# Performance work log

Measured on AMD Instinct MI355X. Metric: run time of the kernel, lower is better.

The kernel has to match this reference:

```python
import jax, jax.numpy as jnp
import numpy as np

KERNEL_SIZE = 16
STRIDE = 8
NEG = -1.0e9


def setup_inputs() -> dict:
    key = jax.random.key(0)
    k1, k2, k3, k4, k5 = jax.random.split(key, 5)
    B, C, L = 8, 512, 4096
    x = jax.random.normal(k1, (B, C, L), dtype=jnp.float32)
    mask = jax.random.randint(k2, (B, L), 0, 2).astype(bool)
    W = jax.random.normal(k3, (C, C), dtype=jnp.float32) * 0.02
    b = jax.random.normal(k4, (C,), dtype=jnp.float32) * 0.02
    v = jax.random.normal(k5, (C,), dtype=jnp.float32) * 0.02
    return {"x": x, "mask": mask, "W": W, "b": b, "v": v}


def reference(x, mask, W, b, v):
    # x: [B, C, L], mask: [B, L] (True = masked out)
    B, C, L = x.shape
    win, step = KERNEL_SIZE, STRIDE
    L_pool = 1 + (L - win) // step
    # per-token projection (identical across windows since proj is per-token)
    h = jnp.tanh(jnp.einsum('bcl,dc->bld', x, W) + b)      # [B, L, C]
    s = jnp.einsum('bld,d->bl', h, v)                       # [B, L]
    idx = jnp.arange(L_pool)[:, None] * step + jnp.arange(win)[None, :]
    sw = s[:, idx]
    mw = mask[:, idx]
    sw = jnp.where(mw, NEG, sw)
    w = jax.nn.softmax(sw, axis=-1)
    w = jnp.where(mw, 0.0, w)
    norm = jnp.clip(jnp.sum(w, axis=-1, keepdims=True), 1e-6, None)
    w = w / norm
    xw = x[:, :, idx]
    return jnp.einsum('bcpw,bpw->bcp', xw, w)               # [B, C, L_pool]
```

## Files before the change

kernel.cpp:

```cpp
#include <hip/hip_runtime.h>
#include <hip/hip_bf16.h>
#include <cmath>

#define Bsz 8
#define Csz 512
#define Lsz 4096
#define LPOOL 511
#define NEGV -1000000000.0f

typedef __attribute__((ext_vector_type(8))) short short8;
typedef __attribute__((ext_vector_type(4))) float float4v;

__device__ __forceinline__ float bf2f(short u) {
  unsigned int x = ((unsigned int)(unsigned short)u) << 16;
  return __builtin_bit_cast(float, x);
}

__device__ __forceinline__ void gl_lds16(const __hip_bfloat16* g, void* l) {
  __builtin_amdgcn_global_load_lds(
      (const __attribute__((address_space(1))) unsigned int*)g,
      (__attribute__((address_space(3))) unsigned int*)l, 16, 0, 0);
}

__global__ __launch_bounds__(256) void stage1(const float* __restrict__ x,
    __hip_bfloat16* __restrict__ xTs, __hip_bfloat16* __restrict__ xbf,
    const unsigned char* __restrict__ mb, int* __restrict__ flag,
    float* __restrict__ s, const float* __restrict__ W,
    __hip_bfloat16* __restrict__ Wts) {
  const int tid = threadIdx.x;
  const int bid = blockIdx.x;
  if (bid < 4096) {
    __shared__ float sX[64][65];
    const int lt = bid & 63, ct = (bid >> 6) & 7, b = bid >> 9;
    const int l0 = lt * 64;
    const float* xb = x + ((size_t)b * Csz + ct * 64) * Lsz + l0;
    #pragma unroll
    for (int it = 0; it < 4; ++it) {
      int c = it * 16 + (tid >> 4);
      int l = (tid & 15) * 4;
      *(float4*)(&sX[c][l]) = *(const float4*)(xb + (size_t)c * Lsz + l);
    }
    __syncthreads();
    #pragma unroll
    for (int it = 0; it < 2; ++it) {
      int u = it * 256 + tid;
      int cg = u >> 6, ll = u & 63;
      __hip_bfloat16 hb[8];
      #pragma unroll
      for (int j = 0; j < 8; ++j)
        hb[j] = __float2bfloat16(sX[cg * 8 + j][ll]);
      int m = b * Lsz + l0 + ll;
      int mt = m >> 7, row = m & 127;
      int cglob = ct * 64 + cg * 8;
      int ks = cglob >> 5, seg = (cglob >> 3) & 3;
      *(short8*)(xTs + (((size_t)mt * 16 + ks) * 512 + seg * 128 + row) * 8) = *(short8*)hb;
    }
    #pragma unroll
    for (int it = 0; it < 2; ++it) {
      int u = it * 256 + tid;
      int cg = u >> 3, lseg = u & 7;
      __hip_bfloat16 hb[8];
      #pragma unroll
      for (int j = 0; j < 8; ++j)
        hb[j] = __float2bfloat16(sX[cg][lseg * 8 + j]);
      *(short8*)(xbf + ((size_t)b * Csz + ct * 64 + cg) * Lsz + l0 + lseg * 8) = *(short8*)hb;
    }
  } else {
    const int pb = bid - 4096;
    if (pb == 0) {
      __shared__ int sf;
      if (tid == 0) sf = 0;
      __syncthreads();
      int f = 0;
      for (int i = tid; i < 4096; i += 256)
        if ((i & 3) && mb[i]) f = 1;
      if (f) atomicOr(&sf, 1);
      __syncthreads();
      if (tid == 0) *flag = sf;
    } else if (pb <= 32) {
      int i = (pb - 1) * 1024 + tid * 4;
      float4 z; z.x = z.y = z.z = z.w = 0.f;
      *(float4*)(s + i) = z;
    } else {
      int tg = (pb - 33) * 256 + tid;
      int d = tg >> 6, cg = tg & 63;
      float4 w0 = *(const float4*)(W + (size_t)d * 512 + cg * 8);
      float4 w1 = *(const float4*)(W + (size_t)d * 512 + cg * 8 + 4);
      __hip_bfloat16 hb[8];
      hb[0] = __float2bfloat16(w0.x); hb[1] = __float2bfloat16(w0.y);
      hb[2] = __float2bfloat16(w0.z); hb[3] = __float2bfloat16(w0.w);
      hb[4] = __float2bfloat16(w1.x); hb[5] = __float2bfloat16(w1.y);
      hb[6] = __float2bfloat16(w1.z); hb[7] = __float2bfloat16(w1.w);
      int nt = d >> 7, row = d & 127, ks = cg >> 2, seg = cg & 3;
      *(short8*)(Wts + (((size_t)nt * 16 + ks) * 512 + seg * 128 + row) * 8) = *(short8*)hb;
    }
  }
}

__global__ __launch_bounds__(256, 2) void gemm_bf16(
    const __hip_bfloat16* __restrict__ xTs, const __hip_bfloat16* __restrict__ Wts,
    const float* __restrict__ bias, const float* __restrict__ v,
    float* __restrict__ s) {
  __shared__ short8 sAv[512];
  __shared__ short8 sBv[512];
  const int tid = threadIdx.x;
  const int lane = tid & 63, wave = tid >> 6;
  const int lr = lane & 15, quad = lane >> 4;
  const int mh = wave >> 1, nh = wave & 1;
  const int mt = blockIdx.x, nt = blockIdx.y;
  const __hip_bfloat16* aT = xTs + (size_t)mt * 65536;
  const __hip_bfloat16* bT = Wts + (size_t)nt * 65536;

  float bl[4], vl[4];
  #pragma unroll
  for (int nf = 0; nf < 4; ++nf) {
    int n = nt * 128 + nh * 64 + nf * 16 + lr;
    bl[nf] = bias[n]; vl[nf] = v[n];
  }

  float4v acc[4][4];
  #pragma unroll
  for (int i = 0; i < 4; ++i)
    #pragma unroll
    for (int j = 0; j < 4; ++j) acc[i][j] = (float4v)0.f;

  for (int ks = 0; ks < 16; ++ks) {
    __syncthreads();
    const __hip_bfloat16* ga = aT + ks * 4096 + (wave * 64 + lane) * 8;
    const __hip_bfloat16* gb = bT + ks * 4096 + (wave * 64 + lane) * 8;
    gl_lds16(ga,        &sAv[wave * 64]);
    gl_lds16(ga + 2048, &sAv[256 + wave * 64]);
    gl_lds16(gb,        &sBv[wave * 64]);
    gl_lds16(gb + 2048, &sBv[256 + wave * 64]);
    __syncthreads();
    short8 af[4], bfr[4];
    #pragma unroll
    for (int mf = 0; mf < 4; ++mf)
      af[mf] = sAv[quad * 128 + mh * 64 + mf * 16 + lr];
    #pragma unroll
    for (int nf = 0; nf < 4; ++nf)
      bfr[nf] = sBv[quad * 128 + nh * 64 + nf * 16 + lr];
    #pragma unroll
    for (int mf = 0; mf < 4; ++mf)
      #pragma unroll
      for (int nf = 0; nf < 4; ++nf)
        acc[mf][nf] = __builtin_amdgcn_mfma_f32_16x16x32_bf16(af[mf], bfr[nf], acc[mf][nf], 0, 0, 0);
  }

  #pragma unroll
  for (int mf = 0; mf < 4; ++mf) {
    #pragma unroll
    for (int reg = 0; reg < 4; ++reg) {
      float p = 0.f;
      #pragma unroll
      for (int nf = 0; nf < 4; ++nf)
        p += tanhf(acc[mf][nf][reg] + bl[nf]) * vl[nf];
      p += __shfl_xor(p, 1, 16);
      p += __shfl_xor(p, 2, 16);
      p += __shfl_xor(p, 4, 16);
      p += __shfl_xor(p, 8, 16);
      if (lr == 0)
        atomicAdd(&s[mt * 128 + mh * 64 + mf * 16 + quad * 4 + reg], p);
    }
  }
}

__global__ __launch_bounds__(256) void pool2(const __hip_bfloat16* __restrict__ xbf,
    const float* __restrict__ s, const void* __restrict__ mask,
    const int* __restrict__ flag, float* __restrict__ out) {
  __shared__ float wl[8][17];
  const int t = threadIdx.x;
  const int p0 = blockIdx.x * 8, b = blockIdx.y;
  if (t < 8 && p0 + t < LPOOL) {
    const int p = p0 + t;
    const bool u8 = (*flag != 0);
    const unsigned char* m8 = (const unsigned char*)mask;
    const int* m32 = (const int*)mask;
    const int base = b * Lsz + p * 8;
    float sv[16]; int mv[16];
    float mx = -3.4e38f;
    #pragma unroll
    for (int w = 0; w < 16; ++w) {
      int mk = u8 ? (int)m8[base + w] : m32[base + w];
      float val = mk ? NEGV : s[base + w];
      sv[w] = val; mv[w] = mk;
      mx = fmaxf(mx, val);
    }
    float sum = 0.f;
    #pragma unroll
    for (int w = 0; w < 16; ++w) { sv[w] = expf(sv[w] - mx); sum += sv[w]; }
    float inv = 1.0f / sum;
    float norm = 0.f;
    #pragma unroll
    for (int w = 0; w < 16; ++w) { sv[w] = mv[w] ? 0.f : sv[w] * inv; norm += sv[w]; }
    norm = fmaxf(norm, 1e-6f);
    float rn = 1.0f / norm;
    #pragma unroll
    for (int w = 0; w < 16; ++w) wl[t][w] = sv[w] * rn;
  }
  __syncthreads();
  const int ci = t >> 3, pi = t & 7;
  const int p = p0 + pi;
  if (p >= LPOOL) return;
  float wr[16];
  #pragma unroll
  for (int w = 0; w < 16; ++w) wr[w] = wl[pi][w];
  #pragma unroll 4
  for (int it = 0; it < 16; ++it) {
    int c = it * 32 + ci;
    const __hip_bfloat16* xp = xbf + ((size_t)b * Csz + c) * Lsz + 8 * p;
    short8 lo = *(const short8*)xp;
    short8 hi = *(const short8*)(xp + 8);
    float acc = 0.f;
    #pragma unroll
    for (int j = 0; j < 8; ++j)
      acc += bf2f(lo[j]) * wr[j] + bf2f(hi[j]) * wr[8 + j];
    out[((size_t)b * Csz + c) * LPOOL + p] = acc;
  }
}

__global__ void detect_mask(const unsigned char* __restrict__ mb, int* __restrict__ flag) {
  __shared__ int sf;
  int t = threadIdx.x;
  if (t == 0) sf = 0;
  __syncthreads();
  int f = 0;
  for (int i = t; i < 4096; i += 256)
    if ((i & 3) && mb[i]) f = 1;
  if (f) atomicOr(&sf, 1);
  __syncthreads();
  if (t == 0) *flag = sf;
}

__global__ __launch_bounds__(256) void gemm_s_f32(const float* __restrict__ x,
    const float* __restrict__ W, const float* __restrict__ bias,
    const float* __restrict__ v, float* __restrict__ s_out) {
  __shared__ float sA[32][64];
  __shared__ float sB[32][68];
  __shared__ float s_acc[64];
  const int tid = threadIdx.x;
  const int b = blockIdx.y;
  const int l0 = blockIdx.x * 64;
  if (tid < 64) s_acc[tid] = 0.0f;
  const int tx = tid & 15;
  const int ty = tid >> 4;
  const float* xb = x + ((size_t)b * Csz) * Lsz + l0;
  for (int d0 = 0; d0 < Csz; d0 += 64) {
    float acc[4][4] = {{0.f}};
    for (int c0 = 0; c0 < Csz; c0 += 32) {
      __syncthreads();
      #pragma unroll
      for (int it = 0; it < 8; ++it) {
        int idx = tid + it * 256;
        int kc = idx >> 6, ml = idx & 63;
        sA[kc][ml] = xb[(size_t)(c0 + kc) * Lsz + ml];
      }
      #pragma unroll
      for (int it = 0; it < 8; ++it) {
        int idx = tid + it * 256;
        int kc = idx & 31, dj = idx >> 5;
        sB[kc][dj] = W[(size_t)(d0 + dj) * Csz + c0 + kc];
      }
      __syncthreads();
      #pragma unroll
      for (int kc = 0; kc < 32; ++kc) {
        float4 a  = *(const float4*)(&sA[kc][tx << 2]);
        float4 w4 = *(const float4*)(&sB[kc][ty << 2]);
        acc[0][0] += a.x * w4.x; acc[0][1] += a.x * w4.y; acc[0][2] += a.x * w4.z; acc[0][3] += a.x * w4.w;
        acc[1][0] += a.y * w4.x; acc[1][1] += a.y * w4.y; acc[1][2] += a.y * w4.z; acc[1][3] += a.y * w4.w;
        acc[2][0] += a.z * w4.x; acc[2][1] += a.z * w4.y; acc[2][2] += a.z * w4.z; acc[2][3] += a.z * w4.w;
        acc[3][0] += a.w * w4.x; acc[3][1] += a.w * w4.y; acc[3][2] += a.w * w4.z; acc[3][3] += a.w * w4.w;
      }
    }
    float part[4] = {0.f, 0.f, 0.f, 0.f};
    #pragma unroll
    for (int j = 0; j < 4; ++j) {
      int d = d0 + (ty << 2) + j;
      float bj = bias[d], vj = v[d];
      #pragma unroll
      for (int i = 0; i < 4; ++i)
        part[i] += tanhf(acc[i][j] + bj) * vj;
    }
    #pragma unroll
    for (int i = 0; i < 4; ++i)
      atomicAdd(&s_acc[(tx << 2) + i], part[i]);
  }
  __syncthreads();
  if (tid < 64) s_out[(size_t)b * Lsz + l0 + tid] = s_acc[tid];
}

__global__ void win_weights(const float* __restrict__ s, const void* __restrict__ mask,
                            const int* __restrict__ flag, float* __restrict__ wgt) {
  int t = blockIdx.x * blockDim.x + threadIdx.x;
  if (t >= Bsz * LPOOL) return;
  int b = t / LPOOL, p = t - b * LPOOL;
  const bool u8 = (*flag != 0);
  const unsigned char* m8 = (const unsigned char*)mask;
  const int* m32 = (const int*)mask;
  float sv[16]; int mv[16];
  float mx = -3.4e38f;
  int base = b * Lsz + p * 8;
  #pragma unroll
  for (int w = 0; w < 16; ++w) {
    int mk = u8 ? (int)m8[base + w] : m32[base + w];
    float val = mk ? NEGV : s[base + w];
    sv[w] = val; mv[w] = mk;
    mx = fmaxf(mx, val);
  }
  float sum = 0.f;
  #pragma unroll
  for (int w = 0; w < 16; ++w) { sv[w] = expf(sv[w] - mx); sum += sv[w]; }
  float inv = 1.0f / sum;
  float norm = 0.f;
  #pragma unroll
  for (int w = 0; w < 16; ++w) { sv[w] = mv[w] ? 0.f : sv[w] * inv; norm += sv[w]; }
  norm = fmaxf(norm, 1e-6f);
  float rn = 1.0f / norm;
  #pragma unroll
  for (int w = 0; w < 16; ++w) wgt[t * 16 + w] = sv[w] * rn;
}

__global__ __launch_bounds__(256) void pool_out(const float* __restrict__ x,
    const float* __restrict__ wgt, float* __restrict__ out) {
  __shared__ float xrow[Lsz];
  int bc = blockIdx.x;
  int c = bc & (Csz - 1);
  int b = bc >> 9;
  const float* xr = x + ((size_t)b * Csz + c) * Lsz;
  int tid = threadIdx.x;
  #pragma unroll
  for (int it = 0; it < 4; ++it) {
    int idx = (tid + it * 256) << 2;
    *(float4*)(&xrow[idx]) = *(const float4*)(&xr[idx]);
  }
  __syncthreads();
  const float* wb = wgt + (size_t)b * LPOOL * 16;
  float* ob = out + ((size_t)b * Csz + c) * LPOOL;
  for (int p = tid; p < LPOOL; p += 256) {
    const float4* wp = (const float4*)(wb + p * 16);
    const float4* xp = (const float4*)(&xrow[p * 8]);
    float acc = 0.f;
    #pragma unroll
    for (int q = 0; q < 4; ++q) {
      float4 wv = wp[q], xv = xp[q];
      acc += xv.x * wv.x + xv.y * wv.y + xv.z * wv.z + xv.w * wv.w;
    }
    ob[p] = acc;
  }
}

extern "C" void kernel_launch(void* const* d_in, const int* in_sizes, int n_in,
                              void* d_out, int out_size, void* d_ws, size_t ws_size,
                              hipStream_t stream) {
  const float* x    = (const float*)d_in[0];
  const void*  mask = d_in[1];
  const float* W    = (const float*)d_in[2];
  const float* bias = (const float*)d_in[3];
  const float* v    = (const float*)d_in[4];
  float* out = (float*)d_out;

  char* wsb = (char*)d_ws;
  int*   flag = (int*)wsb;
  float* s    = (float*)(wsb + 256);
  float* wgt  = (float*)(wsb + 131328);
  __hip_bfloat16* Wts = (__hip_bfloat16*)(wsb + 393216);
  __hip_bfloat16* xTs = (__hip_bfloat16*)(wsb + 917504);
  __hip_bfloat16* xbf = (__hip_bfloat16*)(wsb + 917504 + 33554432);
  const size_t NEED = 917504 + 33554432 + 33554432;

  if (ws_size >= NEED) {
    stage1<<<4096 + 161, 256, 0, stream>>>(x, xTs, xbf,
        (const unsigned char*)mask, flag, s, W, Wts);
    gemm_bf16<<<dim3(256, 4), 256, 0, stream>>>(xTs, Wts, bias, v, s);
    pool2<<<dim3(64, Bsz), 256, 0, stream>>>(xbf, s, mask, flag, out);
  } else {
    detect_mask<<<1, 256, 0, stream>>>((const unsigned char*)mask, flag);
    gemm_s_f32<<<dim3(Lsz / 64, Bsz), 256, 0, stream>>>(x, W, bias, v, s);
    win_weights<<<(Bsz * LPOOL + 255) / 256, 256, 0, stream>>>(s, mask, flag, wgt);
    pool_out<<<Bsz * Csz, 256, 0, stream>>>(x, wgt, out);
  }
}
```

Before: 158.8 us.

## Compute full N per GEMM block and reduce scores in shared memory

The GEMM now uses 512-thread blocks that each cover all 512 output channels for a 128-row tile. The A tile is loaded once instead of four times across N-tiles. Score partials are accumulated with LDS atomics and written directly, so the zero-init of s in stage1 and the global atomics go away. In exchange there are more accumulators per thread (4x8 MFMA tiles), which raises register pressure, and the grid is smaller at 256 blocks.

After: 169.6 us. 1.07x slower.

```diff
diff --git a/kernel.cpp b/kernel.cpp
--- a/kernel.cpp
+++ b/kernel.cpp
@@ -25,8 +25,7 @@
 __global__ __launch_bounds__(256) void stage1(const float* __restrict__ x,
     __hip_bfloat16* __restrict__ xTs, __hip_bfloat16* __restrict__ xbf,
     const unsigned char* __restrict__ mb, int* __restrict__ flag,
-    float* __restrict__ s, const float* __restrict__ W,
-    __hip_bfloat16* __restrict__ Wts) {
+    const float* __restrict__ W, __hip_bfloat16* __restrict__ Wts) {
   const int tid = threadIdx.x;
   const int bid = blockIdx.x;
   if (bid < 4096) {
@@ -77,12 +76,8 @@
       if (f) atomicOr(&sf, 1);
       __syncthreads();
       if (tid == 0) *flag = sf;
-    } else if (pb <= 32) {
-      int i = (pb - 1) * 1024 + tid * 4;
-      float4 z; z.x = z.y = z.z = z.w = 0.f;
-      *(float4*)(s + i) = z;
     } else {
-      int tg = (pb - 33) * 256 + tid;
+      int tg = (pb - 1) * 256 + tid;
       int d = tg >> 6, cg = tg & 63;
       float4 w0 = *(const float4*)(W + (size_t)d * 512 + cg * 8);
       float4 w1 = *(const float4*)(W + (size_t)d * 512 + cg * 8 + 4);
@@ -97,72 +92,81 @@
   }
 }
 
-__global__ __launch_bounds__(256, 2) void gemm_bf16(
+__global__ __launch_bounds__(512, 2) void gemm_bf16(
     const __hip_bfloat16* __restrict__ xTs, const __hip_bfloat16* __restrict__ Wts,
     const float* __restrict__ bias, const float* __restrict__ v,
     float* __restrict__ s) {
   __shared__ short8 sAv[512];
-  __shared__ short8 sBv[512];
+  __shared__ short8 sBv[2048];
+  __shared__ float s_acc[128];
   const int tid = threadIdx.x;
   const int lane = tid & 63, wave = tid >> 6;
   const int lr = lane & 15, quad = lane >> 4;
-  const int mh = wave >> 1, nh = wave & 1;
-  const int mt = blockIdx.x, nt = blockIdx.y;
+  const int mh = wave & 1, nq = wave >> 1;
+  const int mt = blockIdx.x;
   const __hip_bfloat16* aT = xTs + (size_t)mt * 65536;
-  const __hip_bfloat16* bT = Wts + (size_t)nt * 65536;
-
-  float bl[4], vl[4];
-  #pragma unroll
-  for (int nf = 0; nf < 4; ++nf) {
-    int n = nt * 128 + nh * 64 + nf * 16 + lr;
+
+  if (tid < 128) s_acc[tid] = 0.f;
+
+  float bl[8], vl[8];
+  #pragma unroll
+  for (int nf = 0; nf < 8; ++nf) {
+    int n = nq * 128 + nf * 16 + lr;
     bl[nf] = bias[n]; vl[nf] = v[n];
   }
 
-  float4v acc[4][4];
+  float4v acc[4][8];
   #pragma unroll
   for (int i = 0; i < 4; ++i)
     #pragma unroll
-    for (int j = 0; j < 4; ++j) acc[i][j] = (float4v)0.f;
+    for (int j = 0; j < 8; ++j) acc[i][j] = (float4v)0.f;
 
   for (int ks = 0; ks < 16; ++ks) {
     __syncthreads();
-    const __hip_bfloat16* ga = aT + ks * 4096 + (wave * 64 + lane) * 8;
-    const __hip_bfloat16* gb = bT + ks * 4096 + (wave * 64 + lane) * 8;
-    gl_lds16(ga,        &sAv[wave * 64]);
-    gl_lds16(ga + 2048, &sAv[256 + wave * 64]);
-    gl_lds16(gb,        &sBv[wave * 64]);
-    gl_lds16(gb + 2048, &sBv[256 + wave * 64]);
+    gl_lds16(aT + (size_t)ks * 4096 + (size_t)(wave * 64 + lane) * 8,
+             &sAv[wave * 64]);
+    #pragma unroll
+    for (int it = 0; it < 4; ++it) {
+      int job = wave * 4 + it;
+      int nt = job >> 3, seg = (job >> 1) & 3, half = job & 1;
+      const __hip_bfloat16* gb = Wts +
+          (((size_t)nt * 16 + ks) * 512 + seg * 128 + half * 64 + lane) * 8;
+      gl_lds16(gb, &sBv[seg * 512 + nt * 128 + half * 64]);
+    }
     __syncthreads();
-    short8 af[4], bfr[4];
+    short8 af[4], bfr[8];
     #pragma unroll
     for (int mf = 0; mf < 4; ++mf)
       af[mf] = sAv[quad * 128 + mh * 64 + mf * 16 + lr];
     #pragma unroll
-    for (int nf = 0; nf < 4; ++nf)
-      bfr[nf] = sBv[quad * 128 + nh * 64 + nf * 16 + lr];
+    for (int nf = 0; nf < 8; ++nf)
+      bfr[nf] = sBv[quad * 512 + nq * 128 + nf * 16 + lr];
     #pragma unroll
     for (int mf = 0; mf < 4; ++mf)
       #pragma unroll
-      for (int nf = 0; nf < 4; ++nf)
+      for (int nf = 0; nf < 8; ++nf)
         acc[mf][nf] = __builtin_amdgcn_mfma_f32_16x16x32_bf16(af[mf], bfr[nf], acc[mf][nf], 0, 0, 0);
   }
 
+  __syncthreads();
   #pragma unroll
   for (int mf = 0; mf < 4; ++mf) {
     #pragma unroll
     for (int reg = 0; reg < 4; ++reg) {
       float p = 0.f;
       #pragma unroll
-      for (int nf = 0; nf < 4; ++nf)
+      for (int nf = 0; nf < 8; ++nf)
         p += tanhf(acc[mf][nf][reg] + bl[nf]) * vl[nf];
       p += __shfl_xor(p, 1, 16);
       p += __shfl_xor(p, 2, 16);
       p += __shfl_xor(p, 4, 16);
       p += __shfl_xor(p, 8, 16);
       if (lr == 0)
-        atomicAdd(&s[mt * 128 + mh * 64 + mf * 16 + quad * 4 + reg], p);
-    }
-  }
+        atomicAdd(&s_acc[mh * 64 + mf * 16 + quad * 4 + reg], p);
+    }
+  }
+  __syncthreads();
+  if (tid < 128) s[mt * 128 + tid] = s_acc[tid];
 }
 
 __global__ __launch_bounds__(256) void pool2(const __hip_bfloat16* __restrict__ xbf,
@@ -369,9 +373,9 @@
   const size_t NEED = 917504 + 33554432 + 33554432;
 
   if (ws_size >= NEED) {
-    stage1<<<4096 + 161, 256, 0, stream>>>(x, xTs, xbf,
-        (const unsigned char*)mask, flag, s, W, Wts);
-    gemm_bf16<<<dim3(256, 4), 256, 0, stream>>>(xTs, Wts, bias, v, s);
+    stage1<<<4096 + 129, 256, 0, stream>>>(x, xTs, xbf,
+        (const unsigned char*)mask, flag, W, Wts);
+    gemm_bf16<<<256, 512, 0, stream>>>(xTs, Wts, bias, v, s);
     pool2<<<dim3(64, Bsz), 256, 0, stream>>>(xbf, s, mask, flag, out);
   } else {
     detect_mask<<<1, 256, 0, stream>>>((const unsigned char*)mask, flag);
```

## Restructure score GEMM tiling with register-loaded W, double-buffered A, and split partial sums

Applied to the files above, without the earlier changes.

The GEMM grid becomes 512x2 blocks, each covering 64 rows and 256 output features. The W fragments are now read straight from global into registers instead of going through LDS, and the x tile is double-buffered in LDS so the next k-slice loads while MFMAs run. Per-block row reductions are gathered in shared memory and written as two plain partial score arrays, with no global atomics. The pooling kernel sums those two partials, which removes the separate zeroing of s in stage1. W is now fetched per wave from global, and the occupancy hint rises to 4 blocks per CU, which may raise register pressure.

New measurement: 161.2 us. Within noise of the previous version (+1.5%).

```diff
diff --git a/kernel.cpp b/kernel.cpp
--- a/kernel.cpp
+++ b/kernel.cpp
@@ -25,8 +25,7 @@
 __global__ __launch_bounds__(256) void stage1(const float* __restrict__ x,
     __hip_bfloat16* __restrict__ xTs, __hip_bfloat16* __restrict__ xbf,
     const unsigned char* __restrict__ mb, int* __restrict__ flag,
-    float* __restrict__ s, const float* __restrict__ W,
-    __hip_bfloat16* __restrict__ Wts) {
+    const float* __restrict__ W, __hip_bfloat16* __restrict__ Wts) {
   const int tid = threadIdx.x;
   const int bid = blockIdx.x;
   if (bid < 4096) {
@@ -77,12 +76,8 @@
       if (f) atomicOr(&sf, 1);
       __syncthreads();
       if (tid == 0) *flag = sf;
-    } else if (pb <= 32) {
-      int i = (pb - 1) * 1024 + tid * 4;
-      float4 z; z.x = z.y = z.z = z.w = 0.f;
-      *(float4*)(s + i) = z;
     } else {
-      int tg = (pb - 33) * 256 + tid;
+      int tg = (pb - 1) * 256 + tid;
       int d = tg >> 6, cg = tg & 63;
       float4 w0 = *(const float4*)(W + (size_t)d * 512 + cg * 8);
       float4 w1 = *(const float4*)(W + (size_t)d * 512 + cg * 8 + 4);
@@ -97,56 +92,64 @@
   }
 }
 
-__global__ __launch_bounds__(256, 2) void gemm_bf16(
+__global__ __launch_bounds__(256, 4) void gemm_bf16(
     const __hip_bfloat16* __restrict__ xTs, const __hip_bfloat16* __restrict__ Wts,
     const float* __restrict__ bias, const float* __restrict__ v,
     float* __restrict__ s) {
-  __shared__ short8 sAv[512];
-  __shared__ short8 sBv[512];
+  __shared__ short8 sA[2][256];
+  __shared__ float s_acc[64];
   const int tid = threadIdx.x;
   const int lane = tid & 63, wave = tid >> 6;
   const int lr = lane & 15, quad = lane >> 4;
-  const int mh = wave >> 1, nh = wave & 1;
-  const int mt = blockIdx.x, nt = blockIdx.y;
-  const __hip_bfloat16* aT = xTs + (size_t)mt * 65536;
-  const __hip_bfloat16* bT = Wts + (size_t)nt * 65536;
+  const int mtp = blockIdx.x, ns = blockIdx.y;
+  const int mt = mtp >> 1, mhalf = mtp & 1;
+  const int nt = 2 * ns + (wave >> 1);
+  const int nh64 = (wave & 1) * 64;
+
+  if (tid < 64) s_acc[tid] = 0.f;
 
   float bl[4], vl[4];
   #pragma unroll
   for (int nf = 0; nf < 4; ++nf) {
-    int n = nt * 128 + nh * 64 + nf * 16 + lr;
+    int n = ns * 256 + wave * 64 + nf * 16 + lr;
     bl[nf] = bias[n]; vl[nf] = v[n];
   }
 
+  const __hip_bfloat16* aBase = xTs +
+      (((size_t)mt * 16) * 512 + wave * 128 + mhalf * 64 + lane) * 8;
+  const short8* bBase = (const short8*)Wts +
+      ((size_t)nt * 16) * 512 + quad * 128 + nh64 + lr;
+
   float4v acc[4][4];
   #pragma unroll
   for (int i = 0; i < 4; ++i)
     #pragma unroll
     for (int j = 0; j < 4; ++j) acc[i][j] = (float4v)0.f;
 
+  gl_lds16(aBase, &sA[0][wave * 64]);
+
+  int buf = 0;
   for (int ks = 0; ks < 16; ++ks) {
     __syncthreads();
-    const __hip_bfloat16* ga = aT + ks * 4096 + (wave * 64 + lane) * 8;
-    const __hip_bfloat16* gb = bT + ks * 4096 + (wave * 64 + lane) * 8;
-    gl_lds16(ga,        &sAv[wave * 64]);
-    gl_lds16(ga + 2048, &sAv[256 + wave * 64]);
-    gl_lds16(gb,        &sBv[wave * 64]);
-    gl_lds16(gb + 2048, &sBv[256 + wave * 64]);
-    __syncthreads();
-    short8 af[4], bfr[4];
+    if (ks < 15)
+      gl_lds16(aBase + (size_t)(ks + 1) * 512 * 8, &sA[buf ^ 1][wave * 64]);
+    short8 bfr[4];
+    #pragma unroll
+    for (int nf = 0; nf < 4; ++nf)
+      bfr[nf] = bBase[(size_t)ks * 512 + nf * 16];
+    short8 af[4];
     #pragma unroll
     for (int mf = 0; mf < 4; ++mf)
-      af[mf] = sAv[quad * 128 + mh * 64 + mf * 16 + lr];
-    #pragma unroll
-    for (int nf = 0; nf < 4; ++nf)
-      bfr[nf] = sBv[quad * 128 + nh * 64 + nf * 16 + lr];
+      af[mf] = sA[buf][quad * 64 + mf * 16 + lr];
     #pragma unroll
     for (int mf = 0; mf < 4; ++mf)
       #pragma unroll
       for (int nf = 0; nf < 4; ++nf)
         acc[mf][nf] = __builtin_amdgcn_mfma_f32_16x16x32_bf16(af[mf], bfr[nf], acc[mf][nf], 0, 0, 0);
-  }
-
+    buf ^= 1;
+  }
+
+  __syncthreads();
   #pragma unroll
   for (int mf = 0; mf < 4; ++mf) {
     #pragma unroll
@@ -160,9 +163,11 @@
       p += __shfl_xor(p, 4, 16);
       p += __shfl_xor(p, 8, 16);
       if (lr == 0)
-        atomicAdd(&s[mt * 128 + mh * 64 + mf * 16 + quad * 4 + reg], p);
-    }
-  }
+        atomicAdd(&s_acc[mf * 16 + quad * 4 + reg], p);
+    }
+  }
+  __syncthreads();
+  if (tid < 64) s[(size_t)ns * 32768 + mtp * 64 + tid] = s_acc[tid];
 }
 
 __global__ __launch_bounds__(256) void pool2(const __hip_bfloat16* __restrict__ xbf,
@@ -182,7 +187,7 @@
     #pragma unroll
     for (int w = 0; w < 16; ++w) {
       int mk = u8 ? (int)m8[base + w] : m32[base + w];
-      float val = mk ? NEGV : s[base + w];
+      float val = mk ? NEGV : (s[base + w] + s[32768 + base + w]);
       sv[w] = val; mv[w] = mk;
       mx = fmaxf(mx, val);
     }
@@ -361,17 +366,17 @@
 
   char* wsb = (char*)d_ws;
   int*   flag = (int*)wsb;
-  float* s    = (float*)(wsb + 256);
-  float* wgt  = (float*)(wsb + 131328);
-  __hip_bfloat16* Wts = (__hip_bfloat16*)(wsb + 393216);
-  __hip_bfloat16* xTs = (__hip_bfloat16*)(wsb + 917504);
-  __hip_bfloat16* xbf = (__hip_bfloat16*)(wsb + 917504 + 33554432);
-  const size_t NEED = 917504 + 33554432 + 33554432;
+  float* s    = (float*)(wsb + 512);
+  float* wgt  = (float*)(wsb + 262656);
+  __hip_bfloat16* Wts = (__hip_bfloat16*)(wsb + 524288);
+  __hip_bfloat16* xTs = (__hip_bfloat16*)(wsb + 1048576);
+  __hip_bfloat16* xbf = (__hip_bfloat16*)(wsb + 1048576 + 33554432);
+  const size_t NEED = 1048576 + 33554432 + 33554432;
 
   if (ws_size >= NEED) {
-    stage1<<<4096 + 161, 256, 0, stream>>>(x, xTs, xbf,
-        (const unsigned char*)mask, flag, s, W, Wts);
-    gemm_bf16<<<dim3(256, 4), 256, 0, stream>>>(xTs, Wts, bias, v, s);
+    stage1<<<4096 + 129, 256, 0, stream>>>(x, xTs, xbf,
+        (const unsigned char*)mask, flag, W, Wts);
+    gemm_bf16<<<dim3(512, 2), 256, 0, stream>>>(xTs, Wts, bias, v, s);
     pool2<<<dim3(64, Bsz), 256, 0, stream>>>(xbf, s, mask, flag, out);
   } else {
     detect_mask<<<1, 256, 0, stream>>>((const unsigned char*)mask, flag);
```
